# Performance work log

Measured on AMD Instinct MI355X. Metric: run time of the kernel, lower is better.

The kernel has to match this reference:

```python
import jax, jax.numpy as jnp
import numpy as np
import math

B, N, D = 128, 50, 256      # batch, segments per piece, cross-attn feature dim
H_CA = 8                    # cross-attention heads
FP, H_AP = 64, 8            # pooling feature dim / heads
S = N * N                   # flattened similarity length (<= 2560 pos-enc cap)
TEMP = 1.0
LN_EPS = 1e-5


def _ln(x, g, b):
    mu = jnp.mean(x, -1, keepdims=True)
    var = jnp.mean((x - mu) ** 2, -1, keepdims=True)
    return (x - mu) * jax.lax.rsqrt(var + LN_EPS) * g + b


def setup_inputs() -> dict:
    key = jax.random.key(0)
    ks = jax.random.split(key, 32)
    w = lambda i, shp, s=0.02: jax.random.normal(ks[i], shp, jnp.float32) * s
    z = lambda shp: jnp.zeros(shp, jnp.float32)
    o = lambda shp: jnp.ones(shp, jnp.float32)
    return {
        "features1": jax.random.normal(ks[0], (B, N, D), jnp.float32),
        "features2": jax.random.normal(ks[1], (B, N, D), jnp.float32),
        # CrossAttention (weights stored (in,out) so x @ W + b)
        "ca_wq": w(2, (D, D)), "ca_bq": z((D,)),
        "ca_wk": w(3, (D, D)), "ca_bk": z((D,)),
        "ca_wv": w(4, (D, D)), "ca_bv": z((D,)),
        "ca_wo": w(5, (D, D)), "ca_bo": z((D,)),
        "ca_ln1_g": o((D,)), "ca_ln1_b": z((D,)),
        "ca_ln2_g": o((D,)), "ca_ln2_b": z((D,)),
        "ca_w1": w(6, (D, 2 * D)), "ca_b1": z((2 * D,)),
        "ca_w2": w(7, (2 * D, D)), "ca_b2": z((D,)),
        # LearnableMetricSimilarity
        "ms_metric": jnp.eye(D, dtype=jnp.float32),
        "ms_wt": w(8, (D, D)), "ms_bt": z((D,)),
        # AttentionPooling
        "ap_wq": w(9, (1, FP)), "ap_bq": z((FP,)),
        "ap_wk": w(10, (1, FP)), "ap_bk": z((FP,)),
        "ap_wv": w(11, (1, FP)), "ap_bv": z((FP,)),
        "ap_pos": w(12, (1, 2560, FP), 0.02),
        "ap_wo": w(13, (FP, FP)), "ap_bo": z((FP,)),
        "ap_ln_g": o((FP,)), "ap_ln_b": z((FP,)),
    }


def reference(features1, features2,
              ca_wq, ca_bq, ca_wk, ca_bk, ca_wv, ca_bv, ca_wo, ca_bo,
              ca_ln1_g, ca_ln1_b, ca_ln2_g, ca_ln2_b,
              ca_w1, ca_b1, ca_w2, ca_b2,
              ms_metric, ms_wt, ms_bt,
              ap_wq, ap_bq, ap_wk, ap_bk, ap_wv, ap_bv,
              ap_pos, ap_wo, ap_bo, ap_ln_g, ap_ln_b):
    hd = D // H_CA

    def attend(fx, fy):
        q = (fx @ ca_wq + ca_bq).reshape(B, N, H_CA, hd)
        k = (fy @ ca_wk + ca_bk).reshape(B, N, H_CA, hd)
        v = (fy @ ca_wv + ca_bv).reshape(B, N, H_CA, hd)
        # Faithful to original: tensors stay (B,N,H,hd), so matmul with
        # k.transpose(-2,-1) yields per-position head-vs-head attention (B,N,H,H).
        scores = jnp.einsum('bnhd,bngd->bnhg', q, k) / math.sqrt(hd)
        wts = jax.nn.softmax(scores, axis=-1)  # dropout is identity (eval)
        att = jnp.einsum('bnhg,bngd->bnhd', wts, v).reshape(B, N, D)
        x = _ln(fx + att @ ca_wo + ca_bo, ca_ln1_g, ca_ln1_b)
        ffn = jax.nn.relu(x @ ca_w1 + ca_b1) @ ca_w2 + ca_b2
        return _ln(x + ffn, ca_ln2_g, ca_ln2_b)

    e1 = attend(features1, features2)
    e2 = attend(features2, features1)

    # Learnable metric similarity: Mahalanobis distance via quadratic expansion
    # d_ij = t1_i M t1_i + t2_j M t2_j - 2 t1_i M t2_j  (M symmetrized)
    t1 = e1 @ ms_wt + ms_bt
    t2 = e2 @ ms_wt + ms_bt
    M = (ms_metric + ms_metric.T) * 0.5
    t1M = t1 @ M
    t2M = t2 @ M
    q1 = jnp.sum(t1M * t1, axis=-1)                    # (B,N)
    q2 = jnp.sum(t2M * t2, axis=-1)                    # (B,N)
    cross = jnp.einsum('bnd,bmd->bnm', t1M, t2)        # (B,N,N)
    dist = q1[:, :, None] + q2[:, None, :] - 2.0 * cross
    sim = jnp.exp(jnp.clip(-dist / TEMP, -10.0, 10.0))  # (B,N,N)

    # Attention pooling over flattened similarity matrix
    flat = sim.reshape(B, S, 1)
    pos = ap_pos[:, :S, :]
    hdp = FP // H_AP
    q = (flat @ ap_wq + ap_bq + pos).reshape(B, S, H_AP, hdp)
    k = (flat @ ap_wk + ap_bk + pos).reshape(B, S, H_AP, hdp)
    v = (flat @ ap_wv + ap_bv).reshape(B, S, H_AP, hdp)
    scores = jnp.einsum('bshd,bsgd->bshg', q, k) / math.sqrt(hdp)  # (B,S,H,H)
    wts = jax.nn.softmax(scores, axis=-1)
    att = jnp.einsum('bshg,bsgd->bshd', wts, v).reshape(B, S, FP)
    pooled = jnp.mean(att, axis=1) @ ap_wo + ap_bo     # (B,FP)
    return _ln(pooled, ap_ln_g, ap_ln_b)
```

## Files before the change

### kernel.cpp

```cpp
#include <hip/hip_runtime.h>
#include <cstddef>
#include <cstdint>


namespace esn {

constexpr int kB   = 128;
constexpr int kN   = 50;
constexpr int kR   = kB * kN;
constexpr int kR2  = 2 * kR;
constexpr int kS   = kN * kN;

typedef __attribute__((ext_vector_type(8))) short short8;
typedef __attribute__((ext_vector_type(4))) float f32x4;

__device__ inline ushort f2bf_rn(float v) {
  uint32_t u = __float_as_uint(v);
  uint32_t r = (u + 0x7fffu + ((u >> 16) & 1u)) >> 16;
  return (ushort)r;
}
__device__ inline float bf2f(ushort b) {
  return __uint_as_float(((uint32_t)b) << 16);
}
__device__ inline void split2(float v, ushort& h, ushort& l) {
  h = f2bf_rn(v);
  l = f2bf_rn(v - bf2f(h));
}

__device__ __forceinline__ void gld16(const ushort* g, ushort* l) {
  __builtin_amdgcn_global_load_lds(
      (const __attribute__((address_space(1))) void*)g,
      (__attribute__((address_space(3))) void*)l,
      16, 0, 0);
}

template<bool RELU, bool WF32, bool WSPLIT>
__global__ __launch_bounds__(256)
void gemm_mfma_kernel(const ushort* __restrict__ Ah, const ushort* __restrict__ Al, int lda,
                      const ushort* __restrict__ Bh, const ushort* __restrict__ Bl, int ldb,
                      const float* __restrict__ bias,
                      float* __restrict__ C, int ldc,
                      ushort* __restrict__ Ch, ushort* __restrict__ Cl,
                      int K)
{
  __shared__ __align__(16) ushort sAh[2][128 * 32];
  __shared__ __align__(16) ushort sAl[2][128 * 32];
  __shared__ __align__(16) ushort sBh[2][128 * 32];
  __shared__ __align__(16) ushort sBl[2][128 * 32];

  const int tid  = threadIdx.x;
  const int lane = tid & 63;
  const int wave = tid >> 6;
  const int wm   = wave >> 1, wn = wave & 1;
  const int bm   = blockIdx.x * 128, bn = blockIdx.y * 128;

  const int lrow  = lane >> 2;
  const int lslot = lane & 3;

  f32x4 acc[4][4] = {};

  auto stage = [&](int buf, int kt) {
    const int kk = kt << 5;
#pragma unroll
    for (int i = 0; i < 2; i++) {
      const int grp  = wave * 32 + i * 16;
      const int row  = grp + lrow;
      const int c    = lslot ^ ((row >> 1) & 3);
      const size_t aoff = (size_t)(bm + row) * lda + kk + c * 8;
      const size_t boff = (size_t)(bn + row) * ldb + kk + c * 8;
      gld16(Ah + aoff, &sAh[buf][grp * 32]);
      gld16(Al + aoff, &sAl[buf][grp * 32]);
      gld16(Bh + boff, &sBh[buf][grp * 32]);
      gld16(Bl + boff, &sBl[buf][grp * 32]);
    }
  };

  const int nK = K >> 5;
  stage(0, 0);
  int cur = 0;
  for (int kt = 0; kt < nK; kt++) {
    __syncthreads();
    if (kt + 1 < nK) stage(cur ^ 1, kt + 1);

    const int r16 = lane & 15, kq = lane >> 4;
    short8 afh[4], afl[4], bfh[4], bfl[4];
#pragma unroll
    for (int f = 0; f < 4; f++) {
      int arow = wm * 64 + f * 16 + r16;
      int sa = kq ^ ((arow >> 1) & 3);
      afh[f] = *(const short8*)(&sAh[cur][arow * 32 + sa * 8]);
      afl[f] = *(const short8*)(&sAl[cur][arow * 32 + sa * 8]);
      int brow = wn * 64 + f * 16 + r16;
      int sb = kq ^ ((brow >> 1) & 3);
      bfh[f] = *(const short8*)(&sBh[cur][brow * 32 + sb * 8]);
      bfl[f] = *(const short8*)(&sBl[cur][brow * 32 + sb * 8]);
    }
#pragma unroll
    for (int mf = 0; mf < 4; mf++)
#pragma unroll
      for (int nf = 0; nf < 4; nf++) {
        acc[mf][nf] = __builtin_amdgcn_mfma_f32_16x16x32_bf16(afh[mf], bfh[nf], acc[mf][nf], 0, 0, 0);
        acc[mf][nf] = __builtin_amdgcn_mfma_f32_16x16x32_bf16(afh[mf], bfl[nf], acc[mf][nf], 0, 0, 0);
        acc[mf][nf] = __builtin_amdgcn_mfma_f32_16x16x32_bf16(afl[mf], bfh[nf], acc[mf][nf], 0, 0, 0);
      }
    cur ^= 1;
  }

  const int r16 = lane & 15, rq = lane >> 4;
#pragma unroll
  for (int nf = 0; nf < 4; nf++) {
    int col = bn + wn * 64 + nf * 16 + r16;
    float bv = bias ? bias[col] : 0.0f;
#pragma unroll
    for (int mf = 0; mf < 4; mf++) {
      int rowb = bm + wm * 64 + mf * 16 + rq * 4;
#pragma unroll
      for (int r = 0; r < 4; r++) {
        float v = acc[mf][nf][r] + bv;
        if (RELU) v = fmaxf(v, 0.0f);
        size_t off = (size_t)(rowb + r) * ldc + col;
        if (WF32) C[off] = v;
        if (WSPLIT) {
          ushort h, l; split2(v, h, l);
          Ch[off] = h; Cl[off] = l;
        }
      }
    }
  }
}

__global__ void prep_w_kernel(const float* __restrict__ wq, const float* __restrict__ wk,
                              const float* __restrict__ wv, const float* __restrict__ bq,
                              const float* __restrict__ bk, const float* __restrict__ bv,
                              const float* __restrict__ wo, const float* __restrict__ w1,
                              const float* __restrict__ w2, const float* __restrict__ wt,
                              const float* __restrict__ msm,
                              ushort* __restrict__ qkvh, ushort* __restrict__ qkvl,
                              ushort* __restrict__ woh,  ushort* __restrict__ wol,
                              ushort* __restrict__ w1h,  ushort* __restrict__ w1l,
                              ushort* __restrict__ w2h,  ushort* __restrict__ w2l,
                              ushort* __restrict__ wth,  ushort* __restrict__ wtl,
                              ushort* __restrict__ msh,  ushort* __restrict__ msl,
                              float* __restrict__ bqkv)
{
  int idx = blockIdx.x * 256 + threadIdx.x;
  if (idx < 768)
    bqkv[idx] = idx < 256 ? bq[idx] : idx < 512 ? bk[idx - 256] : bv[idx - 512];
  float v; ushort *oh, *ol; int off;
  if (idx < 196608) {
    int n = idx >> 8, k = idx & 255;
    v = n < 256 ? wq[k * 256 + n] : n < 512 ? wk[k * 256 + n - 256] : wv[k * 256 + n - 512];
    oh = qkvh; ol = qkvl; off = idx;
  } else if (idx < 262144) {
    int i = idx - 196608; int n = i >> 8, k = i & 255;
    v = wo[k * 256 + n]; oh = woh; ol = wol; off = i;
  } else if (idx < 393216) {
    int i = idx - 262144; int n = i >> 8, k = i & 255;
    v = w1[k * 512 + n]; oh = w1h; ol = w1l; off = i;
  } else if (idx < 524288) {
    int i = idx - 393216; int n = i >> 9, k = i & 511;
    v = w2[k * 256 + n]; oh = w2h; ol = w2l; off = i;
  } else if (idx < 589824) {
    int i = idx - 524288; int n = i >> 8, k = i & 255;
    v = wt[k * 256 + n]; oh = wth; ol = wtl; off = i;
  } else if (idx < 655360) {
    int i = idx - 589824; int n = i >> 8, k = i & 255;
    v = 0.5f * (msm[k * 256 + n] + msm[n * 256 + k]); oh = msh; ol = msl; off = i;
  } else return;
  ushort h, l; split2(v, h, l);
  oh[off] = h; ol[off] = l;
}

__global__ void split_f_kernel(const float* __restrict__ f1, const float* __restrict__ f2,
                               ushort* __restrict__ Fh, ushort* __restrict__ Fl)
{
  int idx = (blockIdx.x * 256 + threadIdx.x) * 4;
  const float* src = idx < kR * 256 ? f1 + idx : f2 + (idx - kR * 256);
  float4 v = *(const float4*)src;
  ushort h, l;
  split2(v.x, h, l); Fh[idx + 0] = h; Fl[idx + 0] = l;
  split2(v.y, h, l); Fh[idx + 1] = h; Fl[idx + 1] = l;
  split2(v.z, h, l); Fh[idx + 2] = h; Fl[idx + 2] = l;
  split2(v.w, h, l); Fh[idx + 3] = h; Fl[idx + 3] = l;
}

__global__ __launch_bounds__(256)
void ca_attn_kernel(const float* __restrict__ P, ushort* __restrict__ Ah,
                    ushort* __restrict__ Al)
{
  const int rib  = threadIdx.x >> 6;
  const int row  = blockIdx.x * 4 + rib;
  const int lane = threadIdx.x & 63;
  const int partner = (row < kR) ? row + kR : row - kR;
  const float* q = P + (size_t)row * 768;
  const float* k = P + (size_t)partner * 768 + 256;
  const float* v = P + (size_t)partner * 768 + 512;
  const int h = lane >> 3, g = lane & 7;

  float s = 0.0f;
#pragma unroll
  for (int i = 0; i < 8; i++) {
    float4 qa = *(const float4*)(q + h * 32 + i * 4);
    float4 ka = *(const float4*)(k + g * 32 + i * 4);
    s = fmaf(qa.x, ka.x, s); s = fmaf(qa.y, ka.y, s);
    s = fmaf(qa.z, ka.z, s); s = fmaf(qa.w, ka.w, s);
  }
  s *= 0.17677669529663687f;

  float mx = s;
#pragma unroll
  for (int d = 1; d < 8; d <<= 1) mx = fmaxf(mx, __shfl_xor(mx, d));
  float e = expf(s - mx);
  float se = e;
#pragma unroll
  for (int d = 1; d < 8; d <<= 1) se += __shfl_xor(se, d);
  float w = e / se;

  __shared__ float lds_w[4][64];
  lds_w[rib][lane] = w;
  __syncthreads();

  const int dc = lane & 7;
  float o[4] = {};
#pragma unroll
  for (int gg = 0; gg < 8; gg++) {
    float wg = lds_w[rib][h * 8 + gg];
    float4 va = *(const float4*)(v + gg * 32 + dc * 4);
    o[0] = fmaf(wg, va.x, o[0]); o[1] = fmaf(wg, va.y, o[1]);
    o[2] = fmaf(wg, va.z, o[2]); o[3] = fmaf(wg, va.w, o[3]);
  }
  size_t base = (size_t)row * 256 + h * 32 + dc * 4;
#pragma unroll
  for (int j = 0; j < 4; j++) {
    ushort hh, ll; split2(o[j], hh, ll);
    Ah[base + j] = hh; Al[base + j] = ll;
  }
}

template<bool WF32>
__global__ __launch_bounds__(256)
void ln_res_kernel(const float* __restrict__ Y, const float* __restrict__ R1,
                   const float* __restrict__ R2, const float* __restrict__ g,
                   const float* __restrict__ b, float* __restrict__ X,
                   ushort* __restrict__ Xh, ushort* __restrict__ Xl)
{
  const int row  = blockIdx.x * 4 + (threadIdx.x >> 6);
  const int lane = threadIdx.x & 63;
  const float* res = (row < kR) ? (R1 + (size_t)row * 256)
                                : (R2 + (size_t)(row - kR) * 256);
  float4 y4 = *(const float4*)(Y + (size_t)row * 256 + lane * 4);
  float4 r4 = *(const float4*)(res + lane * 4);
  float v[4] = {y4.x + r4.x, y4.y + r4.y, y4.z + r4.z, y4.w + r4.w};

  float ssum = v[0] + v[1] + v[2] + v[3];
#pragma unroll
  for (int d = 1; d < 64; d <<= 1) ssum += __shfl_xor(ssum, d);
  float mu = ssum * (1.0f / 256.0f);
  float qq = 0.0f;
#pragma unroll
  for (int j = 0; j < 4; j++) { float dv = v[j] - mu; qq = fmaf(dv, dv, qq); }
#pragma unroll
  for (int d = 1; d < 64; d <<= 1) qq += __shfl_xor(qq, d);
  float rstd = rsqrtf(qq * (1.0f / 256.0f) + 1e-5f);

  float4 g4 = *(const float4*)(g + lane * 4);
  float4 b4 = *(const float4*)(b + lane * 4);
  float o[4];
  o[0] = (v[0] - mu) * rstd * g4.x + b4.x;
  o[1] = (v[1] - mu) * rstd * g4.y + b4.y;
  o[2] = (v[2] - mu) * rstd * g4.z + b4.z;
  o[3] = (v[3] - mu) * rstd * g4.w + b4.w;
  size_t base = (size_t)row * 256 + lane * 4;
  if (WF32) *(float4*)(X + base) = *(float4*)o;
#pragma unroll
  for (int j = 0; j < 4; j++) {
    ushort hh, ll; split2(o[j], hh, ll);
    Xh[base + j] = hh; Xl[base + j] = ll;
  }
}

__global__ __launch_bounds__(256)
void qdot_kernel(const float* __restrict__ T, const float* __restrict__ TM,
                 float* __restrict__ QD)
{
  const int row  = blockIdx.x * 4 + (threadIdx.x >> 6);
  const int lane = threadIdx.x & 63;
  float4 a = *(const float4*)(T  + (size_t)row * 256 + lane * 4);
  float4 b = *(const float4*)(TM + (size_t)row * 256 + lane * 4);
  float s = a.x * b.x + a.y * b.y + a.z * b.z + a.w * b.w;
#pragma unroll
  for (int d = 1; d < 64; d <<= 1) s += __shfl_xor(s, d);
  if (lane == 0) QD[row] = s;
}

__global__ __launch_bounds__(256)
void cross_kernel(const float* __restrict__ T1M, const float* __restrict__ T2,
                  float* __restrict__ CP)
{
  const int b  = blockIdx.x >> 1;
  const int kh = blockIdx.x & 1;
  __shared__ float sA[128][64];
  __shared__ float sB[128][64];
  const int tid = threadIdx.x;
#pragma unroll
  for (int i = 0; i < 8; i++) {
    int slot = tid + i * 256;
    int n  = slot >> 5;
    int k4 = (slot & 31) * 4;
    float4 a = make_float4(0.f, 0.f, 0.f, 0.f), c = a;
    if (n < 50) {
      a = *(const float4*)(T1M + ((size_t)b * 50 + n) * 256 + kh * 128 + k4);
      c = *(const float4*)(T2  + ((size_t)kR + b * 50 + n) * 256 + kh * 128 + k4);
    }
    sA[k4 + 0][n] = a.x; sA[k4 + 1][n] = a.y; sA[k4 + 2][n] = a.z; sA[k4 + 3][n] = a.w;
    sB[k4 + 0][n] = c.x; sB[k4 + 1][n] = c.y; sB[k4 + 2][n] = c.z; sB[k4 + 3][n] = c.w;
  }
  __syncthreads();
  const int tn = tid & 15, tm = tid >> 4;
  const int n0 = tn * 4, m0 = tm * 4;
  float acc[4][4] = {};
  for (int k = 0; k < 128; k++) {
    float4 a4 = *(const float4*)(&sA[k][n0]);
    float4 b4 = *(const float4*)(&sB[k][m0]);
    float a[4] = {a4.x, a4.y, a4.z, a4.w};
    float c[4] = {b4.x, b4.y, b4.z, b4.w};
#pragma unroll
    for (int i = 0; i < 4; i++)
#pragma unroll
      for (int j = 0; j < 4; j++)
        acc[i][j] = fmaf(a[i], c[j], acc[i][j]);
  }
#pragma unroll
  for (int i = 0; i < 4; i++) {
    float* cp = CP + (((size_t)b * 2 + kh) * 64 + n0 + i) * 64 + m0;
    *(float4*)cp = *(float4*)(&acc[i][0]);
  }
}

__global__ void sim_kernel(const float* __restrict__ CP, const float* __restrict__ QD,
                           float* __restrict__ SIM)
{
  int idx = blockIdx.x * 256 + threadIdx.x;
  if (idx >= kB * kS) return;
  int b = idx / kS, s = idx % kS;
  int n = s / kN, m = s % kN;
  float c = CP[(((size_t)b * 2 + 0) * 64 + n) * 64 + m]
          + CP[(((size_t)b * 2 + 1) * 64 + n) * 64 + m];
  float dist = QD[b * kN + n] + QD[kR + b * kN + m] - 2.0f * c;
  float z = -dist;
  z = fminf(fmaxf(z, -10.0f), 10.0f);
  SIM[idx] = expf(z);
}

__global__ __launch_bounds__(256)
void ap_tables_kernel(const float* __restrict__ pos,
                      const float* __restrict__ wq, const float* __restrict__ bq,
                      const float* __restrict__ wk, const float* __restrict__ bk,
                      float2* __restrict__ TT)
{
  int idx = blockIdx.x * 256 + threadIdx.x;
  if (idx >= kS * 64) return;
  int s = idx >> 6, lane = idx & 63;
  int h = lane >> 3, g = lane & 7;
  float t1 = 0.f, t0 = 0.f;
#pragma unroll
  for (int d = 0; d < 8; d++) {
    float a  = wq[h * 8 + d];
    float c  = bq[h * 8 + d] + pos[s * 64 + h * 8 + d];
    float bb = wk[g * 8 + d];
    float e  = bk[g * 8 + d] + pos[s * 64 + g * 8 + d];
    t1 = fmaf(a, e, t1);
    t1 = fmaf(c, bb, t1);
    t0 = fmaf(c, e, t0);
  }
  TT[idx] = make_float2(t1, t0);
}

__global__ __launch_bounds__(256)
void ap_kernel(const float* __restrict__ SIM, const float2* __restrict__ TT,
               const float* __restrict__ wq, const float* __restrict__ wk,
               float* __restrict__ GP)
{
  const int b    = blockIdx.x;
  const int sb   = blockIdx.y;
  const int wave = threadIdx.x >> 6, lane = threadIdx.x & 63;
  const int strip = sb * 4 + wave;
  const int sIdx = lane >> 3;
  const int h    = lane & 7;

  float wqr[8];
#pragma unroll
  for (int d = 0; d < 8; d++) wqr[d] = wq[h * 8 + d];
  float A2[8];
#pragma unroll
  for (int g = 0; g < 8; g++) {
    float a = 0.f;
#pragma unroll
    for (int d = 0; d < 8; d++) a = fmaf(wqr[d], wk[g * 8 + d], a);
    A2[g] = a;
  }
  const float inv8 = 0.35355339059327373f;

  float G0[8] = {}, G1[8] = {};
  const int s0 = strip * 79;
  for (int it = 0; it < 10; it++) {
    int rel = it * 8 + sIdx;
    int s   = s0 + rel;
    bool valid = (rel < 79) && (s < kS);
    int sc = valid ? s : (kS - 1);
    float f = SIM[(size_t)b * kS + sc];
    const float4* tp = (const float4*)(TT + sc * 64 + h * 8);
    float4 t01 = tp[0], t23 = tp[1], t45 = tp[2], t67 = tp[3];
    float f2 = f * f;
    float x[8];
    x[0] = fmaf(f2, A2[0], fmaf(f, t01.x, t01.y)) * inv8;
    x[1] = fmaf(f2, A2[1], fmaf(f, t01.z, t01.w)) * inv8;
    x[2] = fmaf(f2, A2[2], fmaf(f, t23.x, t23.y)) * inv8;
    x[3] = fmaf(f2, A2[3], fmaf(f, t23.z, t23.w)) * inv8;
    x[4] = fmaf(f2, A2[4], fmaf(f, t45.x, t45.y)) * inv8;
    x[5] = fmaf(f2, A2[5], fmaf(f, t45.z, t45.w)) * inv8;
    x[6] = fmaf(f2, A2[6], fmaf(f, t67.x, t67.y)) * inv8;
    x[7] = fmaf(f2, A2[7], fmaf(f, t67.z, t67.w)) * inv8;
    float mx = fmaxf(fmaxf(fmaxf(x[0], x[1]), fmaxf(x[2], x[3])),
                     fmaxf(fmaxf(x[4], x[5]), fmaxf(x[6], x[7])));
    float e[8], se = 0.f;
#pragma unroll
    for (int g = 0; g < 8; g++) { e[g] = __expf(x[g] - mx); se += e[g]; }
    float inv = valid ? (1.0f / se) : 0.0f;
#pragma unroll
    for (int g = 0; g < 8; g++) {
      float w = e[g] * inv;
      G0[g] += w;
      G1[g] = fmaf(w, f, G1[g]);
    }
  }
#pragma unroll
  for (int m = 8; m <= 32; m <<= 1) {
#pragma unroll
    for (int g = 0; g < 8; g++) {
      G0[g] += __shfl_xor(G0[g], m);
      G1[g] += __shfl_xor(G1[g], m);
    }
  }
  if (sIdx == 0) {
    float* gp = GP + (((size_t)b * 32 + strip) * 2) * 64;
#pragma unroll
    for (int g = 0; g < 8; g++) {
      gp[h * 8 + g]      = G1[g];
      gp[64 + h * 8 + g] = G0[g];
    }
  }
}

__global__ __launch_bounds__(64)
void final_kernel(const float* __restrict__ GP, const float* __restrict__ wv,
                  const float* __restrict__ bv, const float* __restrict__ wo,
                  const float* __restrict__ bo, const float* __restrict__ lg,
                  const float* __restrict__ lb, float* __restrict__ out)
{
  const int b = blockIdx.x, j = threadIdx.x;
  float G1 = 0.f, G0 = 0.f;
  for (int st = 0; st < 32; st++) {
    const float* gp = GP + (((size_t)b * 32 + st) * 2) * 64;
    G1 += gp[j];
    G0 += gp[64 + j];
  }
  __shared__ float sg1[64], sg0[64];
  sg1[j] = G1; sg0[j] = G0;
  __syncthreads();
  const int h = j >> 3, d = j & 7;
  float acc = 0.f;
#pragma unroll
  for (int g = 0; g < 8; g++) {
    acc = fmaf(sg1[h * 8 + g], wv[g * 8 + d], acc);
    acc = fmaf(sg0[h * 8 + g], bv[g * 8 + d], acc);
  }
  double pooled = (double)acc / 2500.0;
  __shared__ double sp[64];
  sp[j] = pooled;
  __syncthreads();
  double o = (double)bo[j];
  for (int dd = 0; dd < 64; dd++) o += sp[dd] * (double)wo[dd * 64 + j];
  double ssum = o;
#pragma unroll
  for (int d2 = 1; d2 < 64; d2 <<= 1) ssum += __shfl_xor(ssum, d2);
  double mu = ssum / 64.0;
  double dv = o - mu;
  double qq = dv * dv;
#pragma unroll
  for (int d2 = 1; d2 < 64; d2 <<= 1) qq += __shfl_xor(qq, d2);
  double var = qq / 64.0;
  double r = 1.0 / sqrt(var + 1e-5);
  out[(size_t)b * 64 + j] = (float)(dv * r * (double)lg[j] + (double)lb[j]);
}

}

extern "C" void kernel_launch(void* const* d_in, const int* in_sizes, int n_in,
                              void* d_out, int out_size, void* d_ws, size_t ws_size,
                              hipStream_t stream)
{
  using namespace esn;
  const float* f1      = (const float*)d_in[0];
  const float* f2      = (const float*)d_in[1];
  const float* ca_wq   = (const float*)d_in[2];
  const float* ca_bq   = (const float*)d_in[3];
  const float* ca_wk   = (const float*)d_in[4];
  const float* ca_bk   = (const float*)d_in[5];
  const float* ca_wv   = (const float*)d_in[6];
  const float* ca_bv   = (const float*)d_in[7];
  const float* ca_wo   = (const float*)d_in[8];
  const float* ca_bo   = (const float*)d_in[9];
  const float* ln1_g   = (const float*)d_in[10];
  const float* ln1_b   = (const float*)d_in[11];
  const float* ln2_g   = (const float*)d_in[12];
  const float* ln2_b   = (const float*)d_in[13];
  const float* ca_w1   = (const float*)d_in[14];
  const float* ca_b1   = (const float*)d_in[15];
  const float* ca_w2   = (const float*)d_in[16];
  const float* ca_b2   = (const float*)d_in[17];
  const float* ms_met  = (const float*)d_in[18];
  const float* ms_wt   = (const float*)d_in[19];
  const float* ms_bt   = (const float*)d_in[20];
  const float* ap_wq   = (const float*)d_in[21];
  const float* ap_bq   = (const float*)d_in[22];
  const float* ap_wk   = (const float*)d_in[23];
  const float* ap_bk   = (const float*)d_in[24];
  const float* ap_wv   = (const float*)d_in[25];
  const float* ap_bv   = (const float*)d_in[26];
  const float* ap_pos  = (const float*)d_in[27];
  const float* ap_wo   = (const float*)d_in[28];
  const float* ap_bo   = (const float*)d_in[29];
  const float* ap_ln_g = (const float*)d_in[30];
  const float* ap_ln_b = (const float*)d_in[31];

  float* ws = (float*)d_ws;
  float*  P    = ws;
  ushort* Hh   = (ushort*)(ws);
  ushort* Hl   = (ushort*)(ws + 3276800);
  float*  TM   = ws;
  ushort* Th   = (ushort*)(ws + 3276800);
  ushort* Tl   = (ushort*)(ws + 4915200);
  float*  Tt   = ws + 6553600;
  ushort* S1h  = (ushort*)(ws + 9830400);
  ushort* S1l  = (ushort*)(ws + 11468800);
  float*  X    = ws + 13107200;
  float*  Y    = ws + 16384000;
  float*  CP   = ws + 16384000;
  float*  SIM  = ws + 17432576;
  float*  GP   = ws + 17752576;
  float2* TT   = (float2*)(ws + 18399744);
  float*  QD   = ws + 19660800;
  ushort* Wqh  = (ushort*)(ws + 19673600);
  ushort* Wql  = (ushort*)(ws + 19771904);
  ushort* Woh  = (ushort*)(ws + 19870208);
  ushort* Wol  = (ushort*)(ws + 19902976);
  ushort* W1h  = (ushort*)(ws + 19935744);
  ushort* W1l  = (ushort*)(ws + 20001280);
  ushort* W2h  = (ushort*)(ws + 20066816);
  ushort* W2l  = (ushort*)(ws + 20132352);
  ushort* Wth  = (ushort*)(ws + 20197888);
  ushort* Wtl  = (ushort*)(ws + 20230656);
  ushort* Msh  = (ushort*)(ws + 20263424);
  ushort* Msl  = (ushort*)(ws + 20296192);
  float*  BQKV = ws + 20328960;

  prep_w_kernel<<<2560, 256, 0, stream>>>(ca_wq, ca_wk, ca_wv, ca_bq, ca_bk, ca_bv,
                                          ca_wo, ca_w1, ca_w2, ms_wt, ms_met,
                                          Wqh, Wql, Woh, Wol, W1h, W1l, W2h, W2l,
                                          Wth, Wtl, Msh, Msl, BQKV);
  split_f_kernel<<<3200, 256, 0, stream>>>(f1, f2, S1h, S1l);
  ap_tables_kernel<<<625, 256, 0, stream>>>(ap_pos, ap_wq, ap_bq, ap_wk, ap_bk, TT);
  gemm_mfma_kernel<false, true, false><<<dim3(100, 6), 256, 0, stream>>>(
      S1h, S1l, 256, Wqh, Wql, 256, BQKV, P, 768, nullptr, nullptr, 256);
  ca_attn_kernel<<<kR2 / 4, 256, 0, stream>>>(P, S1h, S1l);
  gemm_mfma_kernel<false, true, false><<<dim3(100, 2), 256, 0, stream>>>(
      S1h, S1l, 256, Woh, Wol, 256, ca_bo, Y, 256, nullptr, nullptr, 256);
  ln_res_kernel<true><<<kR2 / 4, 256, 0, stream>>>(Y, f1, f2, ln1_g, ln1_b, X, S1h, S1l);
  gemm_mfma_kernel<true, false, true><<<dim3(100, 4), 256, 0, stream>>>(
      S1h, S1l, 256, W1h, W1l, 256, ca_b1, nullptr, 512, Hh, Hl, 256);
  gemm_mfma_kernel<false, true, false><<<dim3(100, 2), 256, 0, stream>>>(
      Hh, Hl, 512, W2h, W2l, 512, ca_b2, Y, 256, nullptr, nullptr, 512);
  ln_res_kernel<false><<<kR2 / 4, 256, 0, stream>>>(Y, X, X + (size_t)kR * 256,
                                                    ln2_g, ln2_b, nullptr, S1h, S1l);
  gemm_mfma_kernel<false, true, true><<<dim3(100, 2), 256, 0, stream>>>(
      S1h, S1l, 256, Wth, Wtl, 256, ms_bt, Tt, 256, Th, Tl, 256);
  gemm_mfma_kernel<false, true, false><<<dim3(100, 2), 256, 0, stream>>>(
      Th, Tl, 256, Msh, Msl, 256, nullptr, TM, 256, nullptr, nullptr, 256);
  qdot_kernel<<<kR2 / 4, 256, 0, stream>>>(Tt, TM, QD);
  cross_kernel<<<kB * 2, 256, 0, stream>>>(TM, Tt, CP);
  sim_kernel<<<(kB * kS + 255) / 256, 256, 0, stream>>>(CP, QD, SIM);
  ap_kernel<<<dim3(kB, 8), 256, 0, stream>>>(SIM, TT, ap_wq, ap_wk, GP);
  final_kernel<<<kB, 64, 0, stream>>>(GP, ap_wv, ap_bv, ap_wo, ap_bo,
                                      ap_ln_g, ap_ln_b, (float*)d_out);
}
```

Before: 213.1 us.

## Fuse prep kernels, fold metric into weight GEMM, fuse cross and sim

Merges the weight, feature-split and pooling-table prep into one launch. Precomputes Wt·M so that a single wider GEMM produces both t and tM, which removes the second chained GEMM. The QKV projection is now stored as bf16 hi/lo pairs instead of fp32, and the fp32 copy of the LN1 output is dropped; the LN2 residual is instead reconstructed from the split buffers. The cross-product and similarity kernels are fused so the partial-sum buffer disappears. This cuts launches and memory traffic, at the cost of a serial 256-length dot loop per thread in the prep kernel and fewer cross-kernel blocks.

Result: slower. 250.6 us (+17.6%).

```diff
diff --git a/kernel.cpp b/kernel.cpp
--- a/kernel.cpp
+++ b/kernel.cpp
@@ -25,6 +25,12 @@
 __device__ inline void split2(float v, ushort& h, ushort& l) {
   h = f2bf_rn(v);
   l = f2bf_rn(v - bf2f(h));
+}
+__device__ inline float4 ld4hl(const ushort* ph, const ushort* pl, int off) {
+  ushort4 h = *(const ushort4*)(ph + off);
+  ushort4 l = *(const ushort4*)(pl + off);
+  return make_float4(bf2f(h.x) + bf2f(l.x), bf2f(h.y) + bf2f(l.y),
+                     bf2f(h.z) + bf2f(l.z), bf2f(h.w) + bf2f(l.w));
 }
 
 __device__ __forceinline__ void gld16(const ushort* g, ushort* l) {
@@ -129,79 +135,115 @@
   }
 }
 
-__global__ void prep_w_kernel(const float* __restrict__ wq, const float* __restrict__ wk,
-                              const float* __restrict__ wv, const float* __restrict__ bq,
-                              const float* __restrict__ bk, const float* __restrict__ bv,
-                              const float* __restrict__ wo, const float* __restrict__ w1,
-                              const float* __restrict__ w2, const float* __restrict__ wt,
-                              const float* __restrict__ msm,
-                              ushort* __restrict__ qkvh, ushort* __restrict__ qkvl,
-                              ushort* __restrict__ woh,  ushort* __restrict__ wol,
-                              ushort* __restrict__ w1h,  ushort* __restrict__ w1l,
-                              ushort* __restrict__ w2h,  ushort* __restrict__ w2l,
-                              ushort* __restrict__ wth,  ushort* __restrict__ wtl,
-                              ushort* __restrict__ msh,  ushort* __restrict__ msl,
-                              float* __restrict__ bqkv)
+__global__ void prep_all_kernel(const float* __restrict__ wq, const float* __restrict__ wk,
+                                const float* __restrict__ wv, const float* __restrict__ bq,
+                                const float* __restrict__ bk, const float* __restrict__ bv,
+                                const float* __restrict__ wo, const float* __restrict__ w1,
+                                const float* __restrict__ w2, const float* __restrict__ wt,
+                                const float* __restrict__ bt, const float* __restrict__ msm,
+                                const float* __restrict__ f1, const float* __restrict__ f2,
+                                const float* __restrict__ pos,
+                                const float* __restrict__ awq, const float* __restrict__ abq,
+                                const float* __restrict__ awk, const float* __restrict__ abk,
+                                ushort* __restrict__ qkvh, ushort* __restrict__ qkvl,
+                                ushort* __restrict__ woh,  ushort* __restrict__ wol,
+                                ushort* __restrict__ w1h,  ushort* __restrict__ w1l,
+                                ushort* __restrict__ w2h,  ushort* __restrict__ w2l,
+                                ushort* __restrict__ wt2h, ushort* __restrict__ wt2l,
+                                float* __restrict__ bqkv,  float* __restrict__ bt2,
+                                ushort* __restrict__ S1h,  ushort* __restrict__ S1l,
+                                float2* __restrict__ TT)
 {
   int idx = blockIdx.x * 256 + threadIdx.x;
-  if (idx < 768)
-    bqkv[idx] = idx < 256 ? bq[idx] : idx < 512 ? bk[idx - 256] : bv[idx - 512];
-  float v; ushort *oh, *ol; int off;
   if (idx < 196608) {
     int n = idx >> 8, k = idx & 255;
-    v = n < 256 ? wq[k * 256 + n] : n < 512 ? wk[k * 256 + n - 256] : wv[k * 256 + n - 512];
-    oh = qkvh; ol = qkvl; off = idx;
+    float v = n < 256 ? wq[k * 256 + n] : n < 512 ? wk[k * 256 + n - 256] : wv[k * 256 + n - 512];
+    ushort h, l; split2(v, h, l); qkvh[idx] = h; qkvl[idx] = l;
   } else if (idx < 262144) {
     int i = idx - 196608; int n = i >> 8, k = i & 255;
-    v = wo[k * 256 + n]; oh = woh; ol = wol; off = i;
+    float v = wo[k * 256 + n];
+    ushort h, l; split2(v, h, l); woh[i] = h; wol[i] = l;
   } else if (idx < 393216) {
     int i = idx - 262144; int n = i >> 8, k = i & 255;
-    v = w1[k * 512 + n]; oh = w1h; ol = w1l; off = i;
+    float v = w1[k * 512 + n];
+    ushort h, l; split2(v, h, l); w1h[i] = h; w1l[i] = l;
   } else if (idx < 524288) {
     int i = idx - 393216; int n = i >> 9, k = i & 511;
-    v = w2[k * 256 + n]; oh = w2h; ol = w2l; off = i;
+    float v = w2[k * 256 + n];
+    ushort h, l; split2(v, h, l); w2h[i] = h; w2l[i] = l;
   } else if (idx < 589824) {
     int i = idx - 524288; int n = i >> 8, k = i & 255;
-    v = wt[k * 256 + n]; oh = wth; ol = wtl; off = i;
+    float v = wt[k * 256 + n];
+    ushort h, l; split2(v, h, l); wt2h[i] = h; wt2l[i] = l;
   } else if (idx < 655360) {
     int i = idx - 589824; int n = i >> 8, k = i & 255;
-    v = 0.5f * (msm[k * 256 + n] + msm[n * 256 + k]); oh = msh; ol = msl; off = i;
-  } else return;
-  ushort h, l; split2(v, h, l);
-  oh[off] = h; ol[off] = l;
-}
-
-__global__ void split_f_kernel(const float* __restrict__ f1, const float* __restrict__ f2,
-                               ushort* __restrict__ Fh, ushort* __restrict__ Fl)
-{
-  int idx = (blockIdx.x * 256 + threadIdx.x) * 4;
-  const float* src = idx < kR * 256 ? f1 + idx : f2 + (idx - kR * 256);
-  float4 v = *(const float4*)src;
-  ushort h, l;
-  split2(v.x, h, l); Fh[idx + 0] = h; Fl[idx + 0] = l;
-  split2(v.y, h, l); Fh[idx + 1] = h; Fl[idx + 1] = l;
-  split2(v.z, h, l); Fh[idx + 2] = h; Fl[idx + 2] = l;
-  split2(v.w, h, l); Fh[idx + 3] = h; Fl[idx + 3] = l;
+    float acc = 0.f;
+    for (int j = 0; j < 256; j++)
+      acc = fmaf(wt[k * 256 + j], 0.5f * (msm[j * 256 + n] + msm[n * 256 + j]), acc);
+    ushort h, l; split2(acc, h, l);
+    wt2h[(256 + n) * 256 + k] = h; wt2l[(256 + n) * 256 + k] = l;
+  } else if (idx < 656128) {
+    int c = idx - 655360;
+    bqkv[c] = c < 256 ? bq[c] : c < 512 ? bk[c - 256] : bv[c - 512];
+  } else if (idx < 656640) {
+    int c = idx - 656128;
+    if (c < 256) bt2[c] = bt[c];
+    else {
+      int n = c - 256;
+      float acc = 0.f;
+      for (int j = 0; j < 256; j++)
+        acc = fmaf(bt[j], 0.5f * (msm[j * 256 + n] + msm[n * 256 + j]), acc);
+      bt2[c] = acc;
+    }
+  } else if (idx < 1475840) {
+    int e4 = (idx - 656640) * 4;
+    const float* src = e4 < kR * 256 ? f1 + e4 : f2 + (e4 - kR * 256);
+    float4 v = *(const float4*)src;
+    ushort h, l;
+    split2(v.x, h, l); S1h[e4 + 0] = h; S1l[e4 + 0] = l;
+    split2(v.y, h, l); S1h[e4 + 1] = h; S1l[e4 + 1] = l;
+    split2(v.z, h, l); S1h[e4 + 2] = h; S1l[e4 + 2] = l;
+    split2(v.w, h, l); S1h[e4 + 3] = h; S1l[e4 + 3] = l;
+  } else if (idx < 1635840) {
+    int t = idx - 1475840;
+    int s = t >> 6, lane = t & 63;
+    int h = lane >> 3, g = lane & 7;
+    float t1 = 0.f, t0 = 0.f;
+#pragma unroll
+    for (int d = 0; d < 8; d++) {
+      float a  = awq[h * 8 + d];
+      float c  = abq[h * 8 + d] + pos[s * 64 + h * 8 + d];
+      float bb = awk[g * 8 + d];
+      float e  = abk[g * 8 + d] + pos[s * 64 + g * 8 + d];
+      t1 = fmaf(a, e, t1);
+      t1 = fmaf(c, bb, t1);
+      t0 = fmaf(c, e, t0);
+    }
+    TT[t] = make_float2(t1, t0);
+  }
 }
 
 __global__ __launch_bounds__(256)
-void ca_attn_kernel(const float* __restrict__ P, ushort* __restrict__ Ah,
-                    ushort* __restrict__ Al)
+void ca_attn_kernel(const ushort* __restrict__ Ph, const ushort* __restrict__ Pl,
+                    ushort* __restrict__ Ah, ushort* __restrict__ Al)
 {
   const int rib  = threadIdx.x >> 6;
   const int row  = blockIdx.x * 4 + rib;
   const int lane = threadIdx.x & 63;
   const int partner = (row < kR) ? row + kR : row - kR;
-  const float* q = P + (size_t)row * 768;
-  const float* k = P + (size_t)partner * 768 + 256;
-  const float* v = P + (size_t)partner * 768 + 512;
+  const ushort* qh = Ph + (size_t)row * 768;
+  const ushort* ql = Pl + (size_t)row * 768;
+  const ushort* kh_ = Ph + (size_t)partner * 768 + 256;
+  const ushort* kl_ = Pl + (size_t)partner * 768 + 256;
+  const ushort* vh = Ph + (size_t)partner * 768 + 512;
+  const ushort* vl = Pl + (size_t)partner * 768 + 512;
   const int h = lane >> 3, g = lane & 7;
 
   float s = 0.0f;
 #pragma unroll
   for (int i = 0; i < 8; i++) {
-    float4 qa = *(const float4*)(q + h * 32 + i * 4);
-    float4 ka = *(const float4*)(k + g * 32 + i * 4);
+    float4 qa = ld4hl(qh, ql, h * 32 + i * 4);
+    float4 ka = ld4hl(kh_, kl_, g * 32 + i * 4);
     s = fmaf(qa.x, ka.x, s); s = fmaf(qa.y, ka.y, s);
     s = fmaf(qa.z, ka.z, s); s = fmaf(qa.w, ka.w, s);
   }
@@ -225,7 +267,7 @@
 #pragma unroll
   for (int gg = 0; gg < 8; gg++) {
     float wg = lds_w[rib][h * 8 + gg];
-    float4 va = *(const float4*)(v + gg * 32 + dc * 4);
+    float4 va = ld4hl(vh, vl, gg * 32 + dc * 4);
     o[0] = fmaf(wg, va.x, o[0]); o[1] = fmaf(wg, va.y, o[1]);
     o[2] = fmaf(wg, va.z, o[2]); o[3] = fmaf(wg, va.w, o[3]);
   }
@@ -237,19 +279,25 @@
   }
 }
 
-template<bool WF32>
+template<bool RES_SPLIT>
 __global__ __launch_bounds__(256)
 void ln_res_kernel(const float* __restrict__ Y, const float* __restrict__ R1,
-                   const float* __restrict__ R2, const float* __restrict__ g,
-                   const float* __restrict__ b, float* __restrict__ X,
-                   ushort* __restrict__ Xh, ushort* __restrict__ Xl)
+                   const float* __restrict__ R2,
+                   const ushort* Rh, const ushort* Rl,
+                   const float* __restrict__ g, const float* __restrict__ b,
+                   ushort* Xh, ushort* Xl)
 {
   const int row  = blockIdx.x * 4 + (threadIdx.x >> 6);
   const int lane = threadIdx.x & 63;
-  const float* res = (row < kR) ? (R1 + (size_t)row * 256)
-                                : (R2 + (size_t)(row - kR) * 256);
   float4 y4 = *(const float4*)(Y + (size_t)row * 256 + lane * 4);
-  float4 r4 = *(const float4*)(res + lane * 4);
+  float4 r4;
+  if (RES_SPLIT) {
+    r4 = ld4hl(Rh + (size_t)row * 256, Rl + (size_t)row * 256, lane * 4);
+  } else {
+    const float* res = (row < kR) ? (R1 + (size_t)row * 256)
+                                  : (R2 + (size_t)(row - kR) * 256);
+    r4 = *(const float4*)(res + lane * 4);
+  }
   float v[4] = {y4.x + r4.x, y4.y + r4.y, y4.z + r4.z, y4.w + r4.w};
 
   float ssum = v[0] + v[1] + v[2] + v[3];
@@ -271,7 +319,6 @@
   o[2] = (v[2] - mu) * rstd * g4.z + b4.z;
   o[3] = (v[3] - mu) * rstd * g4.w + b4.w;
   size_t base = (size_t)row * 256 + lane * 4;
-  if (WF32) *(float4*)(X + base) = *(float4*)o;
 #pragma unroll
   for (int j = 0; j < 4; j++) {
     ushort hh, ll; split2(o[j], hh, ll);
@@ -280,13 +327,12 @@
 }
 
 __global__ __launch_bounds__(256)
-void qdot_kernel(const float* __restrict__ T, const float* __restrict__ TM,
-                 float* __restrict__ QD)
+void qdot_kernel(const float* __restrict__ T2X, float* __restrict__ QD)
 {
   const int row  = blockIdx.x * 4 + (threadIdx.x >> 6);
   const int lane = threadIdx.x & 63;
-  float4 a = *(const float4*)(T  + (size_t)row * 256 + lane * 4);
-  float4 b = *(const float4*)(TM + (size_t)row * 256 + lane * 4);
+  float4 a = *(const float4*)(T2X + (size_t)row * 512 + lane * 4);
+  float4 b = *(const float4*)(T2X + (size_t)row * 512 + 256 + lane * 4);
   float s = a.x * b.x + a.y * b.y + a.z * b.z + a.w * b.w;
 #pragma unroll
   for (int d = 1; d < 64; d <<= 1) s += __shfl_xor(s, d);
@@ -294,86 +340,60 @@
 }
 
 __global__ __launch_bounds__(256)
-void cross_kernel(const float* __restrict__ T1M, const float* __restrict__ T2,
-                  float* __restrict__ CP)
-{
-  const int b  = blockIdx.x >> 1;
-  const int kh = blockIdx.x & 1;
+void cross_sim_kernel(const float* __restrict__ T2X, const float* __restrict__ QD,
+                      float* __restrict__ SIM)
+{
+  const int b = blockIdx.x;
   __shared__ float sA[128][64];
   __shared__ float sB[128][64];
   const int tid = threadIdx.x;
-#pragma unroll
-  for (int i = 0; i < 8; i++) {
-    int slot = tid + i * 256;
-    int n  = slot >> 5;
-    int k4 = (slot & 31) * 4;
-    float4 a = make_float4(0.f, 0.f, 0.f, 0.f), c = a;
-    if (n < 50) {
-      a = *(const float4*)(T1M + ((size_t)b * 50 + n) * 256 + kh * 128 + k4);
-      c = *(const float4*)(T2  + ((size_t)kR + b * 50 + n) * 256 + kh * 128 + k4);
-    }
-    sA[k4 + 0][n] = a.x; sA[k4 + 1][n] = a.y; sA[k4 + 2][n] = a.z; sA[k4 + 3][n] = a.w;
-    sB[k4 + 0][n] = c.x; sB[k4 + 1][n] = c.y; sB[k4 + 2][n] = c.z; sB[k4 + 3][n] = c.w;
-  }
-  __syncthreads();
   const int tn = tid & 15, tm = tid >> 4;
   const int n0 = tn * 4, m0 = tm * 4;
   float acc[4][4] = {};
-  for (int k = 0; k < 128; k++) {
-    float4 a4 = *(const float4*)(&sA[k][n0]);
-    float4 b4 = *(const float4*)(&sB[k][m0]);
-    float a[4] = {a4.x, a4.y, a4.z, a4.w};
-    float c[4] = {b4.x, b4.y, b4.z, b4.w};
-#pragma unroll
-    for (int i = 0; i < 4; i++)
-#pragma unroll
-      for (int j = 0; j < 4; j++)
-        acc[i][j] = fmaf(a[i], c[j], acc[i][j]);
-  }
+
+  for (int kh = 0; kh < 2; kh++) {
+#pragma unroll
+    for (int i = 0; i < 8; i++) {
+      int slot = tid + i * 256;
+      int n  = slot >> 5;
+      int k4 = (slot & 31) * 4;
+      float4 a = make_float4(0.f, 0.f, 0.f, 0.f), c = a;
+      if (n < 50) {
+        a = *(const float4*)(T2X + ((size_t)(b * 50 + n)) * 512 + 256 + kh * 128 + k4);
+        c = *(const float4*)(T2X + ((size_t)(kR + b * 50 + n)) * 512 + kh * 128 + k4);
+      }
+      sA[k4 + 0][n] = a.x; sA[k4 + 1][n] = a.y; sA[k4 + 2][n] = a.z; sA[k4 + 3][n] = a.w;
+      sB[k4 + 0][n] = c.x; sB[k4 + 1][n] = c.y; sB[k4 + 2][n] = c.z; sB[k4 + 3][n] = c.w;
+    }
+    __syncthreads();
+    for (int k = 0; k < 128; k++) {
+      float4 a4 = *(const float4*)(&sA[k][n0]);
+      float4 b4 = *(const float4*)(&sB[k][m0]);
+      float a[4] = {a4.x, a4.y, a4.z, a4.w};
+      float c[4] = {b4.x, b4.y, b4.z, b4.w};
+#pragma unroll
+      for (int i = 0; i < 4; i++)
+#pragma unroll
+        for (int j = 0; j < 4; j++)
+          acc[i][j] = fmaf(a[i], c[j], acc[i][j]);
+    }
+    __syncthreads();
+  }
+
 #pragma unroll
   for (int i = 0; i < 4; i++) {
-    float* cp = CP + (((size_t)b * 2 + kh) * 64 + n0 + i) * 64 + m0;
-    *(float4*)cp = *(float4*)(&acc[i][0]);
-  }
-}
-
-__global__ void sim_kernel(const float* __restrict__ CP, const float* __restrict__ QD,
-                           float* __restrict__ SIM)
-{
-  int idx = blockIdx.x * 256 + threadIdx.x;
-  if (idx >= kB * kS) return;
-  int b = idx / kS, s = idx % kS;
-  int n = s / kN, m = s % kN;
-  float c = CP[(((size_t)b * 2 + 0) * 64 + n) * 64 + m]
-          + CP[(((size_t)b * 2 + 1) * 64 + n) * 64 + m];
-  float dist = QD[b * kN + n] + QD[kR + b * kN + m] - 2.0f * c;
-  float z = -dist;
-  z = fminf(fmaxf(z, -10.0f), 10.0f);
-  SIM[idx] = expf(z);
-}
-
-__global__ __launch_bounds__(256)
-void ap_tables_kernel(const float* __restrict__ pos,
-                      const float* __restrict__ wq, const float* __restrict__ bq,
-                      const float* __restrict__ wk, const float* __restrict__ bk,
-                      float2* __restrict__ TT)
-{
-  int idx = blockIdx.x * 256 + threadIdx.x;
-  if (idx >= kS * 64) return;
-  int s = idx >> 6, lane = idx & 63;
-  int h = lane >> 3, g = lane & 7;
-  float t1 = 0.f, t0 = 0.f;
-#pragma unroll
-  for (int d = 0; d < 8; d++) {
-    float a  = wq[h * 8 + d];
-    float c  = bq[h * 8 + d] + pos[s * 64 + h * 8 + d];
-    float bb = wk[g * 8 + d];
-    float e  = bk[g * 8 + d] + pos[s * 64 + g * 8 + d];
-    t1 = fmaf(a, e, t1);
-    t1 = fmaf(c, bb, t1);
-    t0 = fmaf(c, e, t0);
-  }
-  TT[idx] = make_float2(t1, t0);
+    int n = n0 + i;
+    if (n >= 50) continue;
+    float q1 = QD[b * 50 + n];
+#pragma unroll
+    for (int j = 0; j < 4; j++) {
+      int m = m0 + j;
+      if (m >= 50) continue;
+      float dist = q1 + QD[kR + b * 50 + m] - 2.0f * acc[i][j];
+      float z = fminf(fmaxf(-dist, -10.0f), 10.0f);
+      SIM[(size_t)b * kS + n * 50 + m] = __expf(z);
+    }
+  }
 }
 
 __global__ __launch_bounds__(256)
@@ -535,61 +555,53 @@
   const float* ap_ln_b = (const float*)d_in[31];
 
   float* ws = (float*)d_ws;
-  float*  P    = ws;
+  ushort* Ph   = (ushort*)(ws);
+  ushort* Pl   = (ushort*)(ws + 4915200);
   ushort* Hh   = (ushort*)(ws);
-  ushort* Hl   = (ushort*)(ws + 3276800);
-  float*  TM   = ws;
-  ushort* Th   = (ushort*)(ws + 3276800);
-  ushort* Tl   = (ushort*)(ws + 4915200);
-  float*  Tt   = ws + 6553600;
+  ushort* Hl   = (ushort*)(ws + 1638400);
+  float*  T2X  = ws;
   ushort* S1h  = (ushort*)(ws + 9830400);
-  ushort* S1l  = (ushort*)(ws + 11468800);
-  float*  X    = ws + 13107200;
-  float*  Y    = ws + 16384000;
-  float*  CP   = ws + 16384000;
-  float*  SIM  = ws + 17432576;
-  float*  GP   = ws + 17752576;
-  float2* TT   = (float2*)(ws + 18399744);
-  float*  QD   = ws + 19660800;
-  ushort* Wqh  = (ushort*)(ws + 19673600);
-  ushort* Wql  = (ushort*)(ws + 19771904);
-  ushort* Woh  = (ushort*)(ws + 19870208);
-  ushort* Wol  = (ushort*)(ws + 19902976);
-  ushort* W1h  = (ushort*)(ws + 19935744);
-  ushort* W1l  = (ushort*)(ws + 20001280);
-  ushort* W2h  = (ushort*)(ws + 20066816);
-  ushort* W2l  = (ushort*)(ws + 20132352);
-  ushort* Wth  = (ushort*)(ws + 20197888);
-  ushort* Wtl  = (ushort*)(ws + 20230656);
-  ushort* Msh  = (ushort*)(ws + 20263424);
-  ushort* Msl  = (ushort*)(ws + 20296192);
-  float*  BQKV = ws + 20328960;
-
-  prep_w_kernel<<<2560, 256, 0, stream>>>(ca_wq, ca_wk, ca_wv, ca_bq, ca_bk, ca_bv,
-                                          ca_wo, ca_w1, ca_w2, ms_wt, ms_met,
-                                          Wqh, Wql, Woh, Wol, W1h, W1l, W2h, W2l,
-                                          Wth, Wtl, Msh, Msl, BQKV);
-  split_f_kernel<<<3200, 256, 0, stream>>>(f1, f2, S1h, S1l);
-  ap_tables_kernel<<<625, 256, 0, stream>>>(ap_pos, ap_wq, ap_bq, ap_wk, ap_bk, TT);
-  gemm_mfma_kernel<false, true, false><<<dim3(100, 6), 256, 0, stream>>>(
-      S1h, S1l, 256, Wqh, Wql, 256, BQKV, P, 768, nullptr, nullptr, 256);
-  ca_attn_kernel<<<kR2 / 4, 256, 0, stream>>>(P, S1h, S1l);
+  ushort* S1l  = (ushort*)(ws + 10649600);
+  float*  Y    = ws + 11468800;
+  float*  SIM  = ws + 14745600;
+  float*  GP   = ws + 15065600;
+  float2* TT   = (float2*)(ws + 15589888);
+  float*  QD   = ws + 16229888;
+  ushort* Wqh  = (ushort*)(ws + 16242688);
+  ushort* Wql  = (ushort*)(ws + 16340992);
+  ushort* Woh  = (ushort*)(ws + 16439296);
+  ushort* Wol  = (ushort*)(ws + 16472064);
+  ushort* W1h  = (ushort*)(ws + 16504832);
+  ushort* W1l  = (ushort*)(ws + 16570368);
+  ushort* W2h  = (ushort*)(ws + 16635904);
+  ushort* W2l  = (ushort*)(ws + 16701440);
+  ushort* WT2h = (ushort*)(ws + 16766976);
+  ushort* WT2l = (ushort*)(ws + 16832512);
+  float*  BQKV = ws + 16898048;
+  float*  BT2  = ws + 16898816;
+
+  prep_all_kernel<<<6390, 256, 0, stream>>>(
+      ca_wq, ca_wk, ca_wv, ca_bq, ca_bk, ca_bv, ca_wo, ca_w1, ca_w2,
+      ms_wt, ms_bt, ms_met, f1, f2, ap_pos, ap_wq, ap_bq, ap_wk, ap_bk,
+      Wqh, Wql, Woh, Wol, W1h, W1l, W2h, W2l, WT2h, WT2l,
+      BQKV, BT2, S1h, S1l, TT);
+  gemm_mfma_kernel<false, false, true><<<dim3(100, 6), 256, 0, stream>>>(
+      S1h, S1l, 256, Wqh, Wql, 256, BQKV, nullptr, 768, Ph, Pl, 256);
+  ca_attn_kernel<<<kR2 / 4, 256, 0, stream>>>(Ph, Pl, S1h, S1l);
   gemm_mfma_kernel<false, true, false><<<dim3(100, 2), 256, 0, stream>>>(
       S1h, S1l, 256, Woh, Wol, 256, ca_bo, Y, 256, nullptr, nullptr, 256);
-  ln_res_kernel<true><<<kR2 / 4, 256, 0, stream>>>(Y, f1, f2, ln1_g, ln1_b, X, S1h, S1l);
+  ln_res_kernel<false><<<kR2 / 4, 256, 0, stream>>>(Y, f1, f2, nullptr, nullptr,
+                                                    ln1_g, ln1_b, S1h, S1l);
   gemm_mfma_kernel<true, false, true><<<dim3(100, 4), 256, 0, stream>>>(
       S1h, S1l, 256, W1h, W1l, 256, ca_b1, nullptr, 512, Hh, Hl, 256);
   gemm_mfma_kernel<false, true, false><<<dim3(100, 2), 256, 0, stream>>>(
       Hh, Hl, 512, W2h, W2l, 512, ca_b2, Y, 256, nullptr, nullptr, 512);
-  ln_res_kernel<false><<<kR2 / 4, 256, 0, stream>>>(Y, X, X + (size_t)kR * 256,
-                                                    ln2_g, ln2_b, nullptr, S1h, S1l);
-  gemm_mfma_kernel<false, true, true><<<dim3(100, 2), 256, 0, stream>>>(
-      S1h, S1l, 256, Wth, Wtl, 256, ms_bt, Tt, 256, Th, Tl, 256);
-  gemm_mfma_kernel<false, true, false><<<dim3(100, 2), 256, 0, stream>>>(
-      Th, Tl, 256, Msh, Msl, 256, nullptr, TM, 256, nullptr, nullptr, 256);
-  qdot_kernel<<<kR2 / 4, 256, 0, stream>>>(Tt, TM, QD);
-  cross_kernel<<<kB * 2, 256, 0, stream>>>(TM, Tt, CP);
-  sim_kernel<<<(kB * kS + 255) / 256, 256, 0, stream>>>(CP, QD, SIM);
+  ln_res_kernel<true><<<kR2 / 4, 256, 0, stream>>>(Y, nullptr, nullptr, S1h, S1l,
+                                                   ln2_g, ln2_b, S1h, S1l);
+  gemm_mfma_kernel<false, true, false><<<dim3(100, 4), 256, 0, stream>>>(
+      S1h, S1l, 256, WT2h, WT2l, 256, BT2, T2X, 512, nullptr, nullptr, 256);
+  qdot_kernel<<<kR2 / 4, 256, 0, stream>>>(T2X, QD);
+  cross_sim_kernel<<<kB, 256, 0, stream>>>(T2X, QD, SIM);
   ap_kernel<<<dim3(kB, 8), 256, 0, stream>>>(SIM, TT, ap_wq, ap_wk, GP);
   final_kernel<<<kB, 64, 0, stream>>>(GP, ap_wv, ap_bv, ap_wo, ap_bo,
                                       ap_ln_g, ap_ln_b, (float*)d_out);
```
